# Optimization experiments

Hardware: AMD Instinct MI355X
Metric: run time of the kernel (lower is better)

Reference implementation:

```python
import jax, jax.numpy as jnp
import numpy as np

D_MODEL = 512
HIDDEN = 500
NEG_INF = -1e30


def setup_inputs() -> dict:
    key = jax.random.key(0)
    ks = jax.random.split(key, 12)
    N, K, d, L = 256, 1024, D_MODEL, 64
    s = 0.02
    return {
        "span_embs": jax.random.normal(ks[0], (N, d), jnp.float32),
        "knowledge_embs": jax.random.normal(ks[1], (K, d), jnp.float32),
        "span2concepts": jax.random.randint(ks[2], (N, L), 0, K, jnp.int32),
        "lengths": jax.random.randint(ks[3], (N,), 0, L, jnp.int32),
        "Ws": jax.random.normal(ks[4], (d, d), jnp.float32) * s,
        "bs": jnp.zeros((d,), jnp.float32),
        "W1": jax.random.normal(ks[5], (2 * d, HIDDEN), jnp.float32) * s,
        "b1": jnp.zeros((HIDDEN,), jnp.float32),
        "W2": jax.random.normal(ks[6], (HIDDEN, HIDDEN), jnp.float32) * s,
        "b2": jnp.zeros((HIDDEN,), jnp.float32),
        "W3": jax.random.normal(ks[7], (HIDDEN, 1), jnp.float32) * s,
        "b3": jnp.zeros((1,), jnp.float32),
    }


def reference(span_embs, knowledge_embs, span2concepts, lengths, Ws, bs, W1, b1, W2, b2, W3, b3):
    N, d = span_embs.shape
    K = knowledge_embs.shape[0]
    L = span2concepts.shape[1]

    # sentinel concept per candidate (row K of the per-candidate knowledge table)
    sentinel = jax.nn.relu(span_embs @ Ws + bs)  # [N, d]

    # FFNN scorer over concat([span, concept]) for all K+1 pairs.
    # Split W1 so the [N, K+1, 2d] concat is never materialized (same math).
    W1a, W1b = W1[:d], W1[d:]
    span_part = span_embs @ W1a                          # [N, HIDDEN]
    know_part = knowledge_embs @ W1b                     # [K, HIDDEN]
    sent_part = sentinel @ W1b                           # [N, HIDDEN]
    know_full_part = jnp.concatenate(
        [jnp.broadcast_to(know_part[None], (N, K, HIDDEN)), sent_part[:, None, :]], axis=1
    )                                                    # [N, K+1, HIDDEN]
    h = jax.nn.relu(span_part[:, None, :] + know_full_part + b1)
    h = jax.nn.relu(h @ W2 + b2)                         # [N, K+1, HIDDEN]
    scores = (h @ W3 + b3)[..., 0]                       # [N, K+1]

    # ragged gather: per-candidate concept list + sentinel index K, masked softmax
    valid = jnp.arange(L)[None, :] < jnp.maximum(lengths, 1)[:, None]          # [N, L]
    idx = jnp.concatenate([span2concepts, jnp.full((N, 1), K, jnp.int32)], axis=1)  # [N, L+1]
    mask = jnp.concatenate([valid, jnp.ones((N, 1), bool)], axis=1)            # [N, L+1]

    rel_scores = jnp.take_along_axis(scores, idx, axis=1)
    probs = jax.nn.softmax(jnp.where(mask, rel_scores, NEG_INF), axis=-1)      # [N, L+1]

    is_sent = (idx == K)[..., None]                                            # [N, L+1, 1]
    rel_embs = jnp.where(is_sent, sentinel[:, None, :],
                         knowledge_embs[jnp.minimum(idx, K - 1)])              # [N, L+1, d]
    features = jnp.einsum('nl,nld->nd', probs, rel_embs)                       # [N, d]
    return features, probs
```

## Files before the change

### kernel.cpp

```cpp
#include <hip/hip_runtime.h>
#include <math.h>
#include <stdint.h>

#define D 512
#define H 500
#define NSPAN 256
#define KCON 1024
#define L 64

typedef __attribute__((ext_vector_type(8))) short short8;
typedef __attribute__((ext_vector_type(4))) float floatx4;

__device__ __forceinline__ short f2bf(float f) {
    unsigned u = __builtin_bit_cast(unsigned, f);
    return (short)((u + 0x7fffu + ((u >> 16) & 1u)) >> 16);
}

__global__ __launch_bounds__(512) void k_prep(
    const float* __restrict__ W2, const float* __restrict__ Ws,
    const float* __restrict__ W1,
    short* __restrict__ W2bf, short* __restrict__ Wsbf,
    short* __restrict__ W1abf, short* __restrict__ W1bbf) {
    int b = blockIdx.x, tid = threadIdx.x;
    int mb = b >> 6;
    int s = (b & 63) * 512 + tid;
    int kq = s & 3, n = (s >> 2) & 511, kb = s >> 11;
    int k0 = kb * 32 + kq * 8;
    short8 v8;
    #pragma unroll
    for (int i = 0; i < 8; ++i) {
        int k = k0 + i;
        float v;
        if (mb == 0)      v = (k < H && n < H) ? W2[k * H + n] : 0.f;
        else if (mb == 1) v = Ws[k * D + n];
        else if (mb == 2) v = (n < H) ? W1[k * H + n] : 0.f;
        else              v = (n < H) ? W1[(D + k) * H + n] : 0.f;
        v8[i] = f2bf(v);
    }
    short* dst = (mb == 0) ? W2bf : (mb == 1) ? Wsbf : (mb == 2) ? W1abf : W1bbf;
    ((short8*)dst)[s] = v8;
}

__global__ __launch_bounds__(256) void k_mm1(
    const float* __restrict__ span, const float* __restrict__ know,
    const float* __restrict__ bs, const float* __restrict__ b1,
    const short* __restrict__ Wsbf, const short* __restrict__ W1abf,
    const short* __restrict__ W1bbf,
    float* __restrict__ spanb1, float* __restrict__ parts,
    float* __restrict__ sentinel) {
    __shared__ __align__(16) short Asw[16 * 512];
    int b = blockIdx.x, tid = threadIdx.x;
    int wv = tid >> 6, ln = tid & 63;
    int nl = ln & 15, kq = ln >> 4;
    int aoff = nl * 32 + kq * 8;

    if (b < 160) {
        int rg, nh;
        const float* src;
        const short8* B;
        bool is_span = (b < 32);
        if (is_span) { rg = b >> 1; nh = b & 1; src = span + rg * 16 * D;
                       B = (const short8*)W1abf; }
        else { int bb = b - 32; rg = bb >> 1; nh = bb & 1; src = know + rg * 16 * D;
               B = (const short8*)W1bbf; }
        {
            int r = tid >> 4, kb = tid & 15;
            const float* sp = src + r * D + kb * 32;
            short* dst = &Asw[kb * 512 + r * 32];
            #pragma unroll
            for (int i = 0; i < 32; ++i) dst[i] = f2bf(sp[i]);
        }
        __syncthreads();
        floatx4 acc[4];
        #pragma unroll
        for (int t = 0; t < 4; ++t) acc[t] = (floatx4){0.f, 0.f, 0.f, 0.f};
        int tb = nh * 16 + wv * 4;
        int boff = tb * 64 + nl * 4 + kq;
        #pragma unroll 1
        for (int kb = 0; kb < 16; ++kb) {
            short8 a = *(const short8*)&Asw[kb * 512 + aoff];
            short8 bf[4];
            #pragma unroll
            for (int t = 0; t < 4; ++t) bf[t] = B[kb * 2048 + boff + t * 64];
            #pragma unroll
            for (int t = 0; t < 4; ++t)
                acc[t] = __builtin_amdgcn_mfma_f32_16x16x32_bf16(a, bf[t], acc[t], 0, 0, 0);
        }
        #pragma unroll
        for (int t = 0; t < 4; ++t) {
            int col = (tb + t) * 16 + nl;
            if (col < H) {
                if (is_span) {
                    float bc = b1[col];
                    #pragma unroll
                    for (int r = 0; r < 4; ++r)
                        spanb1[(size_t)(rg * 16 + kq * 4 + r) * H + col] = acc[t][r] + bc;
                } else {
                    #pragma unroll
                    for (int r = 0; r < 4; ++r)
                        parts[(size_t)(rg * 16 + kq * 4 + r) * H + col] = acc[t][r];
                }
            }
        }
        return;
    }

    int rg = b - 160;
    const float* src = span + rg * 16 * D;
    {
        int r = tid >> 4, kb = tid & 15;
        const float* sp = src + r * D + kb * 32;
        short* dst = &Asw[kb * 512 + r * 32];
        #pragma unroll
        for (int i = 0; i < 32; ++i) dst[i] = f2bf(sp[i]);
    }
    __syncthreads();
    floatx4 acc[8];
    #pragma unroll
    for (int t = 0; t < 8; ++t) acc[t] = (floatx4){0.f, 0.f, 0.f, 0.f};
    int boff = wv * 8 * 64 + nl * 4 + kq;
    const short8* B1 = (const short8*)Wsbf;
    #pragma unroll 1
    for (int kb = 0; kb < 16; ++kb) {
        short8 a = *(const short8*)&Asw[kb * 512 + aoff];
        short8 bf[8];
        #pragma unroll
        for (int t = 0; t < 8; ++t) bf[t] = B1[kb * 2048 + boff + t * 64];
        #pragma unroll
        for (int t = 0; t < 8; ++t)
            acc[t] = __builtin_amdgcn_mfma_f32_16x16x32_bf16(a, bf[t], acc[t], 0, 0, 0);
    }
    float vbuf[8][4];
    #pragma unroll
    for (int t = 0; t < 8; ++t) {
        int col = (wv * 8 + t) * 16 + nl;
        float bc = bs[col];
        #pragma unroll
        for (int r = 0; r < 4; ++r) {
            float v = fmaxf(acc[t][r] + bc, 0.f);
            vbuf[t][r] = v;
            sentinel[(size_t)(rg * 16 + kq * 4 + r) * D + col] = v;
        }
    }
    __syncthreads();
    #pragma unroll
    for (int t = 0; t < 8; ++t) {
        int col = (wv * 8 + t) * 16 + nl;
        short* d = &Asw[(col >> 5) * 512 + (col & 31)];
        #pragma unroll
        for (int r = 0; r < 4; ++r) d[(kq * 4 + r) * 32] = f2bf(vbuf[t][r]);
    }
    __syncthreads();
    const short8* B2 = (const short8*)W1bbf;
    #pragma unroll
    for (int t = 0; t < 8; ++t) acc[t] = (floatx4){0.f, 0.f, 0.f, 0.f};
    #pragma unroll 1
    for (int kb = 0; kb < 16; ++kb) {
        short8 a = *(const short8*)&Asw[kb * 512 + aoff];
        short8 bf[8];
        #pragma unroll
        for (int t = 0; t < 8; ++t) bf[t] = B2[kb * 2048 + boff + t * 64];
        #pragma unroll
        for (int t = 0; t < 8; ++t)
            acc[t] = __builtin_amdgcn_mfma_f32_16x16x32_bf16(a, bf[t], acc[t], 0, 0, 0);
    }
    #pragma unroll
    for (int t = 0; t < 8; ++t) {
        int col = (wv * 8 + t) * 16 + nl;
        if (col < H) {
            #pragma unroll
            for (int r = 0; r < 4; ++r)
                parts[(size_t)(KCON + rg * 16 + kq * 4 + r) * H + col] = acc[t][r];
        }
    }
}

__global__ __launch_bounds__(512) void k_fused(
    const int* __restrict__ s2c, const int* __restrict__ lengths,
    const float* __restrict__ spanb1, const float* __restrict__ parts,
    const float* __restrict__ sentinel, const short* __restrict__ W2bf,
    const float* __restrict__ b2, const float* __restrict__ W3,
    const float* __restrict__ b3, const float* __restrict__ know,
    float* __restrict__ out_features, float* __restrict__ out_probs) {
    int n = blockIdx.x, tid = threadIdx.x;
    int V = lengths[n];
    V = (V < 1) ? 1 : ((V > 63) ? 63 : V);
    int R = V + 1;
    int nmt = (R + 15) >> 4;

    __shared__ __align__(16) short Asw[16 * 2048];
    __shared__ float red[8][64];
    __shared__ float sscore[64];
    __shared__ float p[L + 1];
    __shared__ int idx[L];
    __shared__ __align__(16) float4 partb[4][128];

    if (tid < L) idx[tid] = s2c[n * L + tid];

    {
        int r = tid >> 4, kb = tid & 15, k0 = kb * 32;
        const float* spn = spanb1 + (size_t)n * H;
        #pragma unroll
        for (int half = 0; half < 2; ++half) {
            int rr = r + half * 32;
            if (rr < nmt * 16) {
                int mt = rr >> 4, m = rr & 15;
                short* dst = &Asw[kb * 2048 + mt * 512 + m * 32];
                if (rr < R) {
                    const float* src = (rr < V)
                        ? parts + (size_t)s2c[n * L + rr] * H
                        : parts + (size_t)(KCON + n) * H;
                    const float4* s4 = (const float4*)(spn + k0);
                    const float4* r4 = (const float4*)(src + k0);
                    #pragma unroll
                    for (int g = 0; g < 8; ++g) {
                        if (k0 + g * 4 < H) {
                            float4 a = s4[g], c = r4[g];
                            dst[g * 4 + 0] = f2bf(fmaxf(a.x + c.x, 0.f));
                            dst[g * 4 + 1] = f2bf(fmaxf(a.y + c.y, 0.f));
                            dst[g * 4 + 2] = f2bf(fmaxf(a.z + c.z, 0.f));
                            dst[g * 4 + 3] = f2bf(fmaxf(a.w + c.w, 0.f));
                        } else {
                            dst[g * 4 + 0] = 0; dst[g * 4 + 1] = 0;
                            dst[g * 4 + 2] = 0; dst[g * 4 + 3] = 0;
                        }
                    }
                } else {
                    #pragma unroll
                    for (int g = 0; g < 8; ++g)
                        *(short4*)&dst[g * 4] = (short4){0, 0, 0, 0};
                }
            }
        }
    }
    __syncthreads();

    int wv = tid >> 6, ln = tid & 63;
    int nl = ln & 15, kq = ln >> 4;
    int aoffb = nl * 32 + kq * 8;
    int boffb = wv * 4 * 64 + nl * 4 + kq;
    floatx4 acc[4][4];
    #pragma unroll
    for (int mt = 0; mt < 4; ++mt)
        #pragma unroll
        for (int t = 0; t < 4; ++t) acc[mt][t] = (floatx4){0.f, 0.f, 0.f, 0.f};

    const short8* B = (const short8*)W2bf;
    #pragma unroll 1
    for (int kb = 0; kb < 16; ++kb) {
        short8 bfr[4];
        #pragma unroll
        for (int t = 0; t < 4; ++t) bfr[t] = B[kb * 2048 + boffb + t * 64];
        #pragma unroll
        for (int mt = 0; mt < 4; ++mt) {
            if (mt < nmt) {
                short8 a = *(const short8*)&Asw[kb * 2048 + mt * 512 + aoffb];
                #pragma unroll
                for (int t = 0; t < 4; ++t)
                    acc[mt][t] = __builtin_amdgcn_mfma_f32_16x16x32_bf16(a, bfr[t], acc[mt][t], 0, 0, 0);
            }
        }
    }

    float b2c[4], w3c[4];
    #pragma unroll
    for (int t = 0; t < 4; ++t) {
        int col = wv * 64 + t * 16 + nl;
        b2c[t] = (col < H) ? b2[col] : 0.f;
        w3c[t] = (col < H) ? W3[col] : 0.f;
    }
    #pragma unroll
    for (int mt = 0; mt < 4; ++mt) {
        if (mt < nmt) {
            #pragma unroll
            for (int r = 0; r < 4; ++r) {
                float v = fmaxf(acc[mt][0][r] + b2c[0], 0.f) * w3c[0]
                        + fmaxf(acc[mt][1][r] + b2c[1], 0.f) * w3c[1]
                        + fmaxf(acc[mt][2][r] + b2c[2], 0.f) * w3c[2]
                        + fmaxf(acc[mt][3][r] + b2c[3], 0.f) * w3c[3];
                v += __shfl_xor(v, 1, 64);
                v += __shfl_xor(v, 2, 64);
                v += __shfl_xor(v, 4, 64);
                v += __shfl_xor(v, 8, 64);
                if (nl == 0) red[wv][mt * 16 + kq * 4 + r] = v;
            }
        }
    }
    __syncthreads();
    if (tid < R) {
        float s = b3[0];
        #pragma unroll
        for (int w = 0; w < 8; ++w) s += red[w][tid];
        sscore[tid] = s;
    }
    __syncthreads();

    if (tid < 64) {
        float sV = sscore[V];
        float val = (tid < V) ? sscore[tid] : -1e30f;
        float m = val;
        #pragma unroll
        for (int off = 32; off > 0; off >>= 1) m = fmaxf(m, __shfl_xor(m, off, 64));
        m = fmaxf(m, sV);
        float e = (tid < V) ? expf(val - m) : 0.f;
        float s = e;
        #pragma unroll
        for (int off = 32; off > 0; off >>= 1) s += __shfl_xor(s, off, 64);
        float eL = expf(sV - m);
        float inv = 1.f / (s + eL);
        p[tid] = e * inv;
        if (tid == 0) p[L] = eL * inv;
    }
    __syncthreads();
    if (tid <= L) out_probs[n * (L + 1) + tid] = p[tid];

    int sub = tid >> 7, c = tid & 127;
    float4 acc4 = {0.f, 0.f, 0.f, 0.f};
    if (sub == 0) {
        float ps = p[L];
        float4 sv = ((const float4*)sentinel)[n * 128 + c];
        acc4.x = ps * sv.x; acc4.y = ps * sv.y; acc4.z = ps * sv.z; acc4.w = ps * sv.w;
    }
    const float4* kn = (const float4*)know;
    for (int l = sub; l < V; l += 4) {
        float pl = p[l];
        float4 v = kn[idx[l] * 128 + c];
        acc4.x = fmaf(pl, v.x, acc4.x); acc4.y = fmaf(pl, v.y, acc4.y);
        acc4.z = fmaf(pl, v.z, acc4.z); acc4.w = fmaf(pl, v.w, acc4.w);
    }
    partb[sub][c] = acc4;
    __syncthreads();
    if (tid < 128) {
        float4 a0 = partb[0][tid], a1 = partb[1][tid];
        float4 a2 = partb[2][tid], a3 = partb[3][tid];
        float4 o;
        o.x = a0.x + a1.x + a2.x + a3.x;
        o.y = a0.y + a1.y + a2.y + a3.y;
        o.z = a0.z + a1.z + a2.z + a3.z;
        o.w = a0.w + a1.w + a2.w + a3.w;
        ((float4*)out_features)[n * 128 + tid] = o;
    }
}

extern "C" void kernel_launch(void* const* d_in, const int* in_sizes, int n_in,
                              void* d_out, int out_size, void* d_ws, size_t ws_size,
                              hipStream_t stream) {
    const float* span = (const float*)d_in[0];
    const float* know = (const float*)d_in[1];
    const int* s2c = (const int*)d_in[2];
    const int* lengths = (const int*)d_in[3];
    const float* Ws = (const float*)d_in[4];
    const float* bs = (const float*)d_in[5];
    const float* W1 = (const float*)d_in[6];
    const float* b1 = (const float*)d_in[7];
    const float* W2 = (const float*)d_in[8];
    const float* b2 = (const float*)d_in[9];
    const float* W3 = (const float*)d_in[10];
    const float* b3 = (const float*)d_in[11];

    float* ws = (float*)d_ws;
    float* spanb1 = ws;
    float* parts = spanb1 + NSPAN * H;
    float* sentinel = parts + (KCON + NSPAN) * H;
    short* W2bf = (short*)(((uintptr_t)(sentinel + NSPAN * D) + 63) & ~(uintptr_t)63);
    short* Wsbf = W2bf + 512 * 512;
    short* W1abf = Wsbf + 512 * 512;
    short* W1bbf = W1abf + 512 * 512;

    float* out_features = (float*)d_out;
    float* out_probs = out_features + NSPAN * D;

    k_prep<<<256, 512, 0, stream>>>(W2, Ws, W1, W2bf, Wsbf, W1abf, W1bbf);
    k_mm1<<<176, 256, 0, stream>>>(span, know, bs, b1, Wsbf, W1abf, W1bbf,
                                   spanb1, parts, sentinel);
    k_fused<<<NSPAN, 512, 0, stream>>>(s2c, lengths, spanb1, parts, sentinel,
                                       W2bf, b2, W3, b3, know,
                                       out_features, out_probs);
}
```

Before: 126.7 us.

## Fuse three kernels into one cooperative kernel with grid-wide syncs

Replaces the prep, first-matmul and fused scoring kernels with a single cooperative kernel of 256 blocks that uses grid.sync between phases. This removes two kernel launch gaps. The mm1 phase is re-tiled to use 512 threads, so each wave now handles fewer column tiles, and the fp32 loads are vectorized as float4. The trade-off is the cost of grid-wide barriers, plus a shared-memory union sized for the largest phase, which may limit occupancy.

After: 299.0 us. 136% more time.

```diff
diff --git a/kernel.cpp b/kernel.cpp
--- a/kernel.cpp
+++ b/kernel.cpp
@@ -1,6 +1,9 @@
 #include <hip/hip_runtime.h>
+#include <hip/hip_cooperative_groups.h>
 #include <math.h>
 #include <stdint.h>
+
+namespace cg = cooperative_groups;
 
 #define D 512
 #define H 500
@@ -16,329 +19,331 @@
     return (short)((u + 0x7fffu + ((u >> 16) & 1u)) >> 16);
 }
 
-__global__ __launch_bounds__(512) void k_prep(
-    const float* __restrict__ W2, const float* __restrict__ Ws,
-    const float* __restrict__ W1,
+struct SharedMem {
+    union {
+        struct {
+            short Asw[16 * 2048];
+            float red[8][64];
+            float sscore[64];
+            float p[L + 1];
+            int idx[L];
+            float4 partb[4][128];
+        } f;
+        struct {
+            short Asw[16 * 512];
+        } m;
+    } u;
+};
+
+__global__ void __launch_bounds__(512) k_all(
+    const float* __restrict__ span, const float* __restrict__ know,
+    const int* __restrict__ s2c, const int* __restrict__ lengths,
+    const float* __restrict__ Ws, const float* __restrict__ bs,
+    const float* __restrict__ W1, const float* __restrict__ b1,
+    const float* __restrict__ W2, const float* __restrict__ b2,
+    const float* __restrict__ W3, const float* __restrict__ b3,
+    float* __restrict__ spanb1, float* __restrict__ parts,
+    float* __restrict__ sentinel,
     short* __restrict__ W2bf, short* __restrict__ Wsbf,
-    short* __restrict__ W1abf, short* __restrict__ W1bbf) {
-    int b = blockIdx.x, tid = threadIdx.x;
-    int mb = b >> 6;
-    int s = (b & 63) * 512 + tid;
-    int kq = s & 3, n = (s >> 2) & 511, kb = s >> 11;
-    int k0 = kb * 32 + kq * 8;
-    short8 v8;
-    #pragma unroll
-    for (int i = 0; i < 8; ++i) {
-        int k = k0 + i;
-        float v;
-        if (mb == 0)      v = (k < H && n < H) ? W2[k * H + n] : 0.f;
-        else if (mb == 1) v = Ws[k * D + n];
-        else if (mb == 2) v = (n < H) ? W1[k * H + n] : 0.f;
-        else              v = (n < H) ? W1[(D + k) * H + n] : 0.f;
-        v8[i] = f2bf(v);
-    }
-    short* dst = (mb == 0) ? W2bf : (mb == 1) ? Wsbf : (mb == 2) ? W1abf : W1bbf;
-    ((short8*)dst)[s] = v8;
-}
-
-__global__ __launch_bounds__(256) void k_mm1(
-    const float* __restrict__ span, const float* __restrict__ know,
-    const float* __restrict__ bs, const float* __restrict__ b1,
-    const short* __restrict__ Wsbf, const short* __restrict__ W1abf,
-    const short* __restrict__ W1bbf,
-    float* __restrict__ spanb1, float* __restrict__ parts,
-    float* __restrict__ sentinel) {
-    __shared__ __align__(16) short Asw[16 * 512];
+    short* __restrict__ W1abf, short* __restrict__ W1bbf,
+    float* __restrict__ out_features, float* __restrict__ out_probs) {
+    cg::grid_group grid = cg::this_grid();
+    __shared__ SharedMem sh;
     int b = blockIdx.x, tid = threadIdx.x;
     int wv = tid >> 6, ln = tid & 63;
     int nl = ln & 15, kq = ln >> 4;
-    int aoff = nl * 32 + kq * 8;
-
-    if (b < 160) {
-        int rg, nh;
+
+    {
+        int mb = b >> 6;
+        int s = (b & 63) * 512 + tid;
+        int skq = s & 3, n = (s >> 2) & 511, kb = s >> 11;
+        int k0 = kb * 32 + skq * 8;
+        short8 v8;
+        #pragma unroll
+        for (int i = 0; i < 8; ++i) {
+            int k = k0 + i;
+            float v;
+            if (mb == 0)      v = (k < H && n < H) ? W2[k * H + n] : 0.f;
+            else if (mb == 1) v = Ws[k * D + n];
+            else if (mb == 2) v = (n < H) ? W1[k * H + n] : 0.f;
+            else              v = (n < H) ? W1[(D + k) * H + n] : 0.f;
+            v8[i] = f2bf(v);
+        }
+        short* dst = (mb == 0) ? W2bf : (mb == 1) ? Wsbf : (mb == 2) ? W1abf : W1bbf;
+        ((short8*)dst)[s] = v8;
+    }
+    __threadfence();
+    grid.sync();
+
+    if (b < 176) {
+        short* Asw = sh.u.m.Asw;
         const float* src;
-        const short8* B;
-        bool is_span = (b < 32);
-        if (is_span) { rg = b >> 1; nh = b & 1; src = span + rg * 16 * D;
-                       B = (const short8*)W1abf; }
-        else { int bb = b - 32; rg = bb >> 1; nh = bb & 1; src = know + rg * 16 * D;
-               B = (const short8*)W1bbf; }
+        int rg, nh = 0, mode;
+        if (b < 32) { mode = 0; rg = b >> 1; nh = b & 1; src = span + rg * 16 * D; }
+        else if (b < 160) { mode = 1; int bb = b - 32; rg = bb >> 1; nh = bb & 1;
+                            src = know + rg * 16 * D; }
+        else { mode = 2; rg = b - 160; src = span + rg * 16 * D; }
+
         {
-            int r = tid >> 4, kb = tid & 15;
-            const float* sp = src + r * D + kb * 32;
-            short* dst = &Asw[kb * 512 + r * 32];
-            #pragma unroll
-            for (int i = 0; i < 32; ++i) dst[i] = f2bf(sp[i]);
-        }
-        __syncthreads();
-        floatx4 acc[4];
+            int r = tid >> 5, kh = tid & 31;
+            const float4* sp = (const float4*)(src + r * D + kh * 16);
+            short* dst = &Asw[(kh >> 1) * 512 + r * 32 + (kh & 1) * 16];
+            #pragma unroll
+            for (int g = 0; g < 4; ++g) {
+                float4 a = sp[g];
+                short4 o = {f2bf(a.x), f2bf(a.y), f2bf(a.z), f2bf(a.w)};
+                ((short4*)dst)[g] = o;
+            }
+        }
+        __syncthreads();
+        int aoff = nl * 32 + kq * 8;
+
+        if (mode < 2) {
+            const short8* B = (const short8*)((mode == 0) ? W1abf : W1bbf);
+            int tb = nh * 16 + wv * 2;
+            int boff = tb * 64 + nl * 4 + kq;
+            floatx4 acc[2];
+            acc[0] = (floatx4){0.f, 0.f, 0.f, 0.f};
+            acc[1] = acc[0];
+            #pragma unroll 1
+            for (int kb = 0; kb < 16; ++kb) {
+                short8 a = *(const short8*)&Asw[kb * 512 + aoff];
+                short8 bf0 = B[kb * 2048 + boff];
+                short8 bf1 = B[kb * 2048 + boff + 64];
+                acc[0] = __builtin_amdgcn_mfma_f32_16x16x32_bf16(a, bf0, acc[0], 0, 0, 0);
+                acc[1] = __builtin_amdgcn_mfma_f32_16x16x32_bf16(a, bf1, acc[1], 0, 0, 0);
+            }
+            #pragma unroll
+            for (int t = 0; t < 2; ++t) {
+                int col = (tb + t) * 16 + nl;
+                if (col < H) {
+                    if (mode == 0) {
+                        float bc = b1[col];
+                        #pragma unroll
+                        for (int r = 0; r < 4; ++r)
+                            spanb1[(size_t)(rg * 16 + kq * 4 + r) * H + col] = acc[t][r] + bc;
+                    } else {
+                        #pragma unroll
+                        for (int r = 0; r < 4; ++r)
+                            parts[(size_t)(rg * 16 + kq * 4 + r) * H + col] = acc[t][r];
+                    }
+                }
+            }
+        } else {
+            int boff = (wv * 4) * 64 + nl * 4 + kq;
+            floatx4 acc[4];
+            #pragma unroll
+            for (int t = 0; t < 4; ++t) acc[t] = (floatx4){0.f, 0.f, 0.f, 0.f};
+            const short8* B1 = (const short8*)Wsbf;
+            #pragma unroll 1
+            for (int kb = 0; kb < 16; ++kb) {
+                short8 a = *(const short8*)&Asw[kb * 512 + aoff];
+                short8 bf[4];
+                #pragma unroll
+                for (int t = 0; t < 4; ++t) bf[t] = B1[kb * 2048 + boff + t * 64];
+                #pragma unroll
+                for (int t = 0; t < 4; ++t)
+                    acc[t] = __builtin_amdgcn_mfma_f32_16x16x32_bf16(a, bf[t], acc[t], 0, 0, 0);
+            }
+            float vbuf[4][4];
+            #pragma unroll
+            for (int t = 0; t < 4; ++t) {
+                int col = (wv * 4 + t) * 16 + nl;
+                float bc = bs[col];
+                #pragma unroll
+                for (int r = 0; r < 4; ++r) {
+                    float v = fmaxf(acc[t][r] + bc, 0.f);
+                    vbuf[t][r] = v;
+                    sentinel[(size_t)(rg * 16 + kq * 4 + r) * D + col] = v;
+                }
+            }
+            __syncthreads();
+            #pragma unroll
+            for (int t = 0; t < 4; ++t) {
+                int col = (wv * 4 + t) * 16 + nl;
+                short* d = &Asw[(col >> 5) * 512 + (col & 31)];
+                #pragma unroll
+                for (int r = 0; r < 4; ++r) d[(kq * 4 + r) * 32] = f2bf(vbuf[t][r]);
+            }
+            __syncthreads();
+            const short8* B2 = (const short8*)W1bbf;
+            #pragma unroll
+            for (int t = 0; t < 4; ++t) acc[t] = (floatx4){0.f, 0.f, 0.f, 0.f};
+            #pragma unroll 1
+            for (int kb = 0; kb < 16; ++kb) {
+                short8 a = *(const short8*)&Asw[kb * 512 + aoff];
+                short8 bf[4];
+                #pragma unroll
+                for (int t = 0; t < 4; ++t) bf[t] = B2[kb * 2048 + boff + t * 64];
+                #pragma unroll
+                for (int t = 0; t < 4; ++t)
+                    acc[t] = __builtin_amdgcn_mfma_f32_16x16x32_bf16(a, bf[t], acc[t], 0, 0, 0);
+            }
+            #pragma unroll
+            for (int t = 0; t < 4; ++t) {
+                int col = (wv * 4 + t) * 16 + nl;
+                if (col < H) {
+                    #pragma unroll
+                    for (int r = 0; r < 4; ++r)
+                        parts[(size_t)(KCON + rg * 16 + kq * 4 + r) * H + col] = acc[t][r];
+                }
+            }
+        }
+    }
+    __threadfence();
+    grid.sync();
+
+    {
+        int n = b;
+        int V = lengths[n];
+        V = (V < 1) ? 1 : ((V > 63) ? 63 : V);
+        int R = V + 1;
+        int nmt = (R + 15) >> 4;
+
+        short* Asw = sh.u.f.Asw;
+        if (tid < L) sh.u.f.idx[tid] = s2c[n * L + tid];
+
+        {
+            int r = tid >> 4, kb = tid & 15, k0 = kb * 32;
+            const float* spn = spanb1 + (size_t)n * H;
+            #pragma unroll
+            for (int half = 0; half < 2; ++half) {
+                int rr = r + half * 32;
+                if (rr < nmt * 16) {
+                    int mt = rr >> 4, m = rr & 15;
+                    short* dst = &Asw[kb * 2048 + mt * 512 + m * 32];
+                    if (rr < R) {
+                        const float* src = (rr < V)
+                            ? parts + (size_t)s2c[n * L + rr] * H
+                            : parts + (size_t)(KCON + n) * H;
+                        const float4* s4 = (const float4*)(spn + k0);
+                        const float4* r4 = (const float4*)(src + k0);
+                        #pragma unroll
+                        for (int g = 0; g < 8; ++g) {
+                            if (k0 + g * 4 < H) {
+                                float4 a = s4[g], c = r4[g];
+                                dst[g * 4 + 0] = f2bf(fmaxf(a.x + c.x, 0.f));
+                                dst[g * 4 + 1] = f2bf(fmaxf(a.y + c.y, 0.f));
+                                dst[g * 4 + 2] = f2bf(fmaxf(a.z + c.z, 0.f));
+                                dst[g * 4 + 3] = f2bf(fmaxf(a.w + c.w, 0.f));
+                            } else {
+                                *(short4*)&dst[g * 4] = (short4){0, 0, 0, 0};
+                            }
+                        }
+                    } else {
+                        #pragma unroll
+                        for (int g = 0; g < 8; ++g)
+                            *(short4*)&dst[g * 4] = (short4){0, 0, 0, 0};
+                    }
+                }
+            }
+        }
+        __syncthreads();
+
+        int aoffb = nl * 32 + kq * 8;
+        int boffb = wv * 4 * 64 + nl * 4 + kq;
+        floatx4 acc[4][4];
         #pragma unroll
-        for (int t = 0; t < 4; ++t) acc[t] = (floatx4){0.f, 0.f, 0.f, 0.f};
-        int tb = nh * 16 + wv * 4;
-        int boff = tb * 64 + nl * 4 + kq;
+        for (int mt = 0; mt < 4; ++mt)
+            #pragma unroll
+            for (int t = 0; t < 4; ++t) acc[mt][t] = (floatx4){0.f, 0.f, 0.f, 0.f};
+
+        const short8* B = (const short8*)W2bf;
         #pragma unroll 1
         for (int kb = 0; kb < 16; ++kb) {
-            short8 a = *(const short8*)&Asw[kb * 512 + aoff];
-            short8 bf[4];
-            #pragma unroll
-            for (int t = 0; t < 4; ++t) bf[t] = B[kb * 2048 + boff + t * 64];
-            #pragma unroll
-            for (int t = 0; t < 4; ++t)
-                acc[t] = __builtin_amdgcn_mfma_f32_16x16x32_bf16(a, bf[t], acc[t], 0, 0, 0);
-        }
+            short8 bfr[4];
+            #pragma unroll
+            for (int t = 0; t < 4; ++t) bfr[t] = B[kb * 2048 + boffb + t * 64];
+            #pragma unroll
+            for (int mt = 0; mt < 4; ++mt) {
+                if (mt < nmt) {
+                    short8 a = *(const short8*)&Asw[kb * 2048 + mt * 512 + aoffb];
+                    #pragma unroll
+                    for (int t = 0; t < 4; ++t)
+                        acc[mt][t] = __builtin_amdgcn_mfma_f32_16x16x32_bf16(a, bfr[t], acc[mt][t], 0, 0, 0);
+                }
+            }
+        }
+
+        float b2c[4], w3c[4];
         #pragma unroll
         for (int t = 0; t < 4; ++t) {
-            int col = (tb + t) * 16 + nl;
-            if (col < H) {
-                if (is_span) {
-                    float bc = b1[col];
-                    #pragma unroll
-                    for (int r = 0; r < 4; ++r)
-                        spanb1[(size_t)(rg * 16 + kq * 4 + r) * H + col] = acc[t][r] + bc;
-                } else {
-                    #pragma unroll
-                    for (int r = 0; r < 4; ++r)
-                        parts[(size_t)(rg * 16 + kq * 4 + r) * H + col] = acc[t][r];
-                }
-            }
-        }
-        return;
-    }
-
-    int rg = b - 160;
-    const float* src = span + rg * 16 * D;
-    {
-        int r = tid >> 4, kb = tid & 15;
-        const float* sp = src + r * D + kb * 32;
-        short* dst = &Asw[kb * 512 + r * 32];
-        #pragma unroll
-        for (int i = 0; i < 32; ++i) dst[i] = f2bf(sp[i]);
-    }
-    __syncthreads();
-    floatx4 acc[8];
-    #pragma unroll
-    for (int t = 0; t < 8; ++t) acc[t] = (floatx4){0.f, 0.f, 0.f, 0.f};
-    int boff = wv * 8 * 64 + nl * 4 + kq;
-    const short8* B1 = (const short8*)Wsbf;
-    #pragma unroll 1
-    for (int kb = 0; kb < 16; ++kb) {
-        short8 a = *(const short8*)&Asw[kb * 512 + aoff];
-        short8 bf[8];
-        #pragma unroll
-        for (int t = 0; t < 8; ++t) bf[t] = B1[kb * 2048 + boff + t * 64];
-        #pragma unroll
-        for (int t = 0; t < 8; ++t)
-            acc[t] = __builtin_amdgcn_mfma_f32_16x16x32_bf16(a, bf[t], acc[t], 0, 0, 0);
-    }
-    float vbuf[8][4];
-    #pragma unroll
-    for (int t = 0; t < 8; ++t) {
-        int col = (wv * 8 + t) * 16 + nl;
-        float bc = bs[col];
-        #pragma unroll
-        for (int r = 0; r < 4; ++r) {
-            float v = fmaxf(acc[t][r] + bc, 0.f);
-            vbuf[t][r] = v;
-            sentinel[(size_t)(rg * 16 + kq * 4 + r) * D + col] = v;
-        }
-    }
-    __syncthreads();
-    #pragma unroll
-    for (int t = 0; t < 8; ++t) {
-        int col = (wv * 8 + t) * 16 + nl;
-        short* d = &Asw[(col >> 5) * 512 + (col & 31)];
-        #pragma unroll
-        for (int r = 0; r < 4; ++r) d[(kq * 4 + r) * 32] = f2bf(vbuf[t][r]);
-    }
-    __syncthreads();
-    const short8* B2 = (const short8*)W1bbf;
-    #pragma unroll
-    for (int t = 0; t < 8; ++t) acc[t] = (floatx4){0.f, 0.f, 0.f, 0.f};
-    #pragma unroll 1
-    for (int kb = 0; kb < 16; ++kb) {
-        short8 a = *(const short8*)&Asw[kb * 512 + aoff];
-        short8 bf[8];
-        #pragma unroll
-        for (int t = 0; t < 8; ++t) bf[t] = B2[kb * 2048 + boff + t * 64];
-        #pragma unroll
-        for (int t = 0; t < 8; ++t)
-            acc[t] = __builtin_amdgcn_mfma_f32_16x16x32_bf16(a, bf[t], acc[t], 0, 0, 0);
-    }
-    #pragma unroll
-    for (int t = 0; t < 8; ++t) {
-        int col = (wv * 8 + t) * 16 + nl;
-        if (col < H) {
-            #pragma unroll
-            for (int r = 0; r < 4; ++r)
-                parts[(size_t)(KCON + rg * 16 + kq * 4 + r) * H + col] = acc[t][r];
-        }
-    }
-}
-
-__global__ __launch_bounds__(512) void k_fused(
-    const int* __restrict__ s2c, const int* __restrict__ lengths,
-    const float* __restrict__ spanb1, const float* __restrict__ parts,
-    const float* __restrict__ sentinel, const short* __restrict__ W2bf,
-    const float* __restrict__ b2, const float* __restrict__ W3,
-    const float* __restrict__ b3, const float* __restrict__ know,
-    float* __restrict__ out_features, float* __restrict__ out_probs) {
-    int n = blockIdx.x, tid = threadIdx.x;
-    int V = lengths[n];
-    V = (V < 1) ? 1 : ((V > 63) ? 63 : V);
-    int R = V + 1;
-    int nmt = (R + 15) >> 4;
-
-    __shared__ __align__(16) short Asw[16 * 2048];
-    __shared__ float red[8][64];
-    __shared__ float sscore[64];
-    __shared__ float p[L + 1];
-    __shared__ int idx[L];
-    __shared__ __align__(16) float4 partb[4][128];
-
-    if (tid < L) idx[tid] = s2c[n * L + tid];
-
-    {
-        int r = tid >> 4, kb = tid & 15, k0 = kb * 32;
-        const float* spn = spanb1 + (size_t)n * H;
-        #pragma unroll
-        for (int half = 0; half < 2; ++half) {
-            int rr = r + half * 32;
-            if (rr < nmt * 16) {
-                int mt = rr >> 4, m = rr & 15;
-                short* dst = &Asw[kb * 2048 + mt * 512 + m * 32];
-                if (rr < R) {
-                    const float* src = (rr < V)
-                        ? parts + (size_t)s2c[n * L + rr] * H
-                        : parts + (size_t)(KCON + n) * H;
-                    const float4* s4 = (const float4*)(spn + k0);
-                    const float4* r4 = (const float4*)(src + k0);
-                    #pragma unroll
-                    for (int g = 0; g < 8; ++g) {
-                        if (k0 + g * 4 < H) {
-                            float4 a = s4[g], c = r4[g];
-                            dst[g * 4 + 0] = f2bf(fmaxf(a.x + c.x, 0.f));
-                            dst[g * 4 + 1] = f2bf(fmaxf(a.y + c.y, 0.f));
-                            dst[g * 4 + 2] = f2bf(fmaxf(a.z + c.z, 0.f));
-                            dst[g * 4 + 3] = f2bf(fmaxf(a.w + c.w, 0.f));
-                        } else {
-                            dst[g * 4 + 0] = 0; dst[g * 4 + 1] = 0;
-                            dst[g * 4 + 2] = 0; dst[g * 4 + 3] = 0;
-                        }
-                    }
-                } else {
-                    #pragma unroll
-                    for (int g = 0; g < 8; ++g)
-                        *(short4*)&dst[g * 4] = (short4){0, 0, 0, 0};
-                }
-            }
-        }
-    }
-    __syncthreads();
-
-    int wv = tid >> 6, ln = tid & 63;
-    int nl = ln & 15, kq = ln >> 4;
-    int aoffb = nl * 32 + kq * 8;
-    int boffb = wv * 4 * 64 + nl * 4 + kq;
-    floatx4 acc[4][4];
-    #pragma unroll
-    for (int mt = 0; mt < 4; ++mt)
-        #pragma unroll
-        for (int t = 0; t < 4; ++t) acc[mt][t] = (floatx4){0.f, 0.f, 0.f, 0.f};
-
-    const short8* B = (const short8*)W2bf;
-    #pragma unroll 1
-    for (int kb = 0; kb < 16; ++kb) {
-        short8 bfr[4];
-        #pragma unroll
-        for (int t = 0; t < 4; ++t) bfr[t] = B[kb * 2048 + boffb + t * 64];
+            int col = wv * 64 + t * 16 + nl;
+            b2c[t] = (col < H) ? b2[col] : 0.f;
+            w3c[t] = (col < H) ? W3[col] : 0.f;
+        }
         #pragma unroll
         for (int mt = 0; mt < 4; ++mt) {
             if (mt < nmt) {
-                short8 a = *(const short8*)&Asw[kb * 2048 + mt * 512 + aoffb];
-                #pragma unroll
-                for (int t = 0; t < 4; ++t)
-                    acc[mt][t] = __builtin_amdgcn_mfma_f32_16x16x32_bf16(a, bfr[t], acc[mt][t], 0, 0, 0);
-            }
-        }
-    }
-
-    float b2c[4], w3c[4];
-    #pragma unroll
-    for (int t = 0; t < 4; ++t) {
-        int col = wv * 64 + t * 16 + nl;
-        b2c[t] = (col < H) ? b2[col] : 0.f;
-        w3c[t] = (col < H) ? W3[col] : 0.f;
-    }
-    #pragma unroll
-    for (int mt = 0; mt < 4; ++mt) {
-        if (mt < nmt) {
-            #pragma unroll
-            for (int r = 0; r < 4; ++r) {
-                float v = fmaxf(acc[mt][0][r] + b2c[0], 0.f) * w3c[0]
-                        + fmaxf(acc[mt][1][r] + b2c[1], 0.f) * w3c[1]
-                        + fmaxf(acc[mt][2][r] + b2c[2], 0.f) * w3c[2]
-                        + fmaxf(acc[mt][3][r] + b2c[3], 0.f) * w3c[3];
-                v += __shfl_xor(v, 1, 64);
-                v += __shfl_xor(v, 2, 64);
-                v += __shfl_xor(v, 4, 64);
-                v += __shfl_xor(v, 8, 64);
-                if (nl == 0) red[wv][mt * 16 + kq * 4 + r] = v;
-            }
-        }
-    }
-    __syncthreads();
-    if (tid < R) {
-        float s = b3[0];
-        #pragma unroll
-        for (int w = 0; w < 8; ++w) s += red[w][tid];
-        sscore[tid] = s;
-    }
-    __syncthreads();
-
-    if (tid < 64) {
-        float sV = sscore[V];
-        float val = (tid < V) ? sscore[tid] : -1e30f;
-        float m = val;
-        #pragma unroll
-        for (int off = 32; off > 0; off >>= 1) m = fmaxf(m, __shfl_xor(m, off, 64));
-        m = fmaxf(m, sV);
-        float e = (tid < V) ? expf(val - m) : 0.f;
-        float s = e;
-        #pragma unroll
-        for (int off = 32; off > 0; off >>= 1) s += __shfl_xor(s, off, 64);
-        float eL = expf(sV - m);
-        float inv = 1.f / (s + eL);
-        p[tid] = e * inv;
-        if (tid == 0) p[L] = eL * inv;
-    }
-    __syncthreads();
-    if (tid <= L) out_probs[n * (L + 1) + tid] = p[tid];
-
-    int sub = tid >> 7, c = tid & 127;
-    float4 acc4 = {0.f, 0.f, 0.f, 0.f};
-    if (sub == 0) {
-        float ps = p[L];
-        float4 sv = ((const float4*)sentinel)[n * 128 + c];
-        acc4.x = ps * sv.x; acc4.y = ps * sv.y; acc4.z = ps * sv.z; acc4.w = ps * sv.w;
-    }
-    const float4* kn = (const float4*)know;
-    for (int l = sub; l < V; l += 4) {
-        float pl = p[l];
-        float4 v = kn[idx[l] * 128 + c];
-        acc4.x = fmaf(pl, v.x, acc4.x); acc4.y = fmaf(pl, v.y, acc4.y);
-        acc4.z = fmaf(pl, v.z, acc4.z); acc4.w = fmaf(pl, v.w, acc4.w);
-    }
-    partb[sub][c] = acc4;
-    __syncthreads();
-    if (tid < 128) {
-        float4 a0 = partb[0][tid], a1 = partb[1][tid];
-        float4 a2 = partb[2][tid], a3 = partb[3][tid];
-        float4 o;
-        o.x = a0.x + a1.x + a2.x + a3.x;
-        o.y = a0.y + a1.y + a2.y + a3.y;
-        o.z = a0.z + a1.z + a2.z + a3.z;
-        o.w = a0.w + a1.w + a2.w + a3.w;
-        ((float4*)out_features)[n * 128 + tid] = o;
+                #pragma unroll
+                for (int r = 0; r < 4; ++r) {
+                    float v = fmaxf(acc[mt][0][r] + b2c[0], 0.f) * w3c[0]
+                            + fmaxf(acc[mt][1][r] + b2c[1], 0.f) * w3c[1]
+                            + fmaxf(acc[mt][2][r] + b2c[2], 0.f) * w3c[2]
+                            + fmaxf(acc[mt][3][r] + b2c[3], 0.f) * w3c[3];
+                    v += __shfl_xor(v, 1, 64);
+                    v += __shfl_xor(v, 2, 64);
+                    v += __shfl_xor(v, 4, 64);
+                    v += __shfl_xor(v, 8, 64);
+                    if (nl == 0) sh.u.f.red[wv][mt * 16 + kq * 4 + r] = v;
+                }
+            }
+        }
+        __syncthreads();
+        if (tid < R) {
+            float s = b3[0];
+            #pragma unroll
+            for (int w = 0; w < 8; ++w) s += sh.u.f.red[w][tid];
+            sh.u.f.sscore[tid] = s;
+        }
+        __syncthreads();
+
+        if (tid < 64) {
+            float sV = sh.u.f.sscore[V];
+            float val = (tid < V) ? sh.u.f.sscore[tid] : -1e30f;
+            float m = val;
+            #pragma unroll
+            for (int off = 32; off > 0; off >>= 1) m = fmaxf(m, __shfl_xor(m, off, 64));
+            m = fmaxf(m, sV);
+            float e = (tid < V) ? expf(val - m) : 0.f;
+            float s = e;
+            #pragma unroll
+            for (int off = 32; off > 0; off >>= 1) s += __shfl_xor(s, off, 64);
+            float eL = expf(sV - m);
+            float inv = 1.f / (s + eL);
+            sh.u.f.p[tid] = e * inv;
+            if (tid == 0) sh.u.f.p[L] = eL * inv;
+        }
+        __syncthreads();
+        if (tid <= L) out_probs[n * (L + 1) + tid] = sh.u.f.p[tid];
+
+        int sub = tid >> 7, c = tid & 127;
+        float4 acc4 = {0.f, 0.f, 0.f, 0.f};
+        if (sub == 0) {
+            float ps = sh.u.f.p[L];
+            float4 sv = ((const float4*)sentinel)[n * 128 + c];
+            acc4.x = ps * sv.x; acc4.y = ps * sv.y;
+            acc4.z = ps * sv.z; acc4.w = ps * sv.w;
+        }
+        const float4* kn = (const float4*)know;
+        for (int l = sub; l < V; l += 4) {
+            float pl = sh.u.f.p[l];
+            float4 v = kn[sh.u.f.idx[l] * 128 + c];
+            acc4.x = fmaf(pl, v.x, acc4.x); acc4.y = fmaf(pl, v.y, acc4.y);
+            acc4.z = fmaf(pl, v.z, acc4.z); acc4.w = fmaf(pl, v.w, acc4.w);
+        }
+        sh.u.f.partb[sub][c] = acc4;
+        __syncthreads();
+        if (tid < 128) {
+            float4 a0 = sh.u.f.partb[0][tid], a1 = sh.u.f.partb[1][tid];
+            float4 a2 = sh.u.f.partb[2][tid], a3 = sh.u.f.partb[3][tid];
+            float4 o;
+            o.x = a0.x + a1.x + a2.x + a3.x;
+            o.y = a0.y + a1.y + a2.y + a3.y;
+            o.z = a0.z + a1.z + a2.z + a3.z;
+            o.w = a0.w + a1.w + a2.w + a3.w;
+            ((float4*)out_features)[n * 128 + tid] = o;
+        }
     }
 }
 
@@ -358,8 +363,8 @@
     const float* W3 = (const float*)d_in[10];
     const float* b3 = (const float*)d_in[11];
 
-    float* ws = (float*)d_ws;
-    float* spanb1 = ws;
+    float* wsp = (float*)d_ws;
+    float* spanb1 = wsp;
     float* parts = spanb1 + NSPAN * H;
     float* sentinel = parts + (KCON + NSPAN) * H;
     short* W2bf = (short*)(((uintptr_t)(sentinel + NSPAN * D) + 63) & ~(uintptr_t)63);
@@ -370,10 +375,14 @@
     float* out_features = (float*)d_out;
     float* out_probs = out_features + NSPAN * D;
 
-    k_prep<<<256, 512, 0, stream>>>(W2, Ws, W1, W2bf, Wsbf, W1abf, W1bbf);
-    k_mm1<<<176, 256, 0, stream>>>(span, know, bs, b1, Wsbf, W1abf, W1bbf,
-                                   spanb1, parts, sentinel);
-    k_fused<<<NSPAN, 512, 0, stream>>>(s2c, lengths, spanb1, parts, sentinel,
-                                       W2bf, b2, W3, b3, know,
-                                       out_features, out_probs);
+    void* args[] = {
+        (void*)&span, (void*)&know, (void*)&s2c, (void*)&lengths,
+        (void*)&Ws, (void*)&bs, (void*)&W1, (void*)&b1,
+        (void*)&W2, (void*)&b2, (void*)&W3, (void*)&b3,
+        (void*)&spanb1, (void*)&parts, (void*)&sentinel,
+        (void*)&W2bf, (void*)&Wsbf, (void*)&W1abf, (void*)&W1bbf,
+        (void*)&out_features, (void*)&out_probs,
+    };
+    hipLaunchCooperativeKernel((void*)k_all, dim3(NSPAN), dim3(512), args, 0,
+                               stream);
 }
```

## Move W2 bf16 conversion into mm1 kernel and prefetch B fragments in MFMA loops

Applied to the files above, without the earlier changes.

Takes the W2-to-bf16 conversion out of the prep kernel and runs it in 128 extra blocks of the mm1 launch, so it overlaps with the first-layer GEMM instead of sitting on the critical path. Both the mm1 and fused W2 MFMA loops now double-buffer the B-fragment global loads, issuing the next k-block's loads before the current MFMAs. The tail zero-fill is also vectorised to a single short4 store. The prefetch adds register pressure, and it wraps around to issue one redundant load on the last iteration.

Result: no change. 125.2 us (-1.1%).

```diff
diff --git a/kernel.cpp b/kernel.cpp
--- a/kernel.cpp
+++ b/kernel.cpp
@@ -17,10 +17,9 @@
 }
 
 __global__ __launch_bounds__(512) void k_prep(
-    const float* __restrict__ W2, const float* __restrict__ Ws,
-    const float* __restrict__ W1,
-    short* __restrict__ W2bf, short* __restrict__ Wsbf,
-    short* __restrict__ W1abf, short* __restrict__ W1bbf) {
+    const float* __restrict__ Ws, const float* __restrict__ W1,
+    short* __restrict__ Wsbf, short* __restrict__ W1abf,
+    short* __restrict__ W1bbf) {
     int b = blockIdx.x, tid = threadIdx.x;
     int mb = b >> 6;
     int s = (b & 63) * 512 + tid;
@@ -31,25 +30,41 @@
     for (int i = 0; i < 8; ++i) {
         int k = k0 + i;
         float v;
-        if (mb == 0)      v = (k < H && n < H) ? W2[k * H + n] : 0.f;
-        else if (mb == 1) v = Ws[k * D + n];
-        else if (mb == 2) v = (n < H) ? W1[k * H + n] : 0.f;
+        if (mb == 0)      v = Ws[k * D + n];
+        else if (mb == 1) v = (n < H) ? W1[k * H + n] : 0.f;
         else              v = (n < H) ? W1[(D + k) * H + n] : 0.f;
         v8[i] = f2bf(v);
     }
-    short* dst = (mb == 0) ? W2bf : (mb == 1) ? Wsbf : (mb == 2) ? W1abf : W1bbf;
+    short* dst = (mb == 0) ? Wsbf : (mb == 1) ? W1abf : W1bbf;
     ((short8*)dst)[s] = v8;
 }
 
 __global__ __launch_bounds__(256) void k_mm1(
     const float* __restrict__ span, const float* __restrict__ know,
     const float* __restrict__ bs, const float* __restrict__ b1,
+    const float* __restrict__ W2,
     const short* __restrict__ Wsbf, const short* __restrict__ W1abf,
     const short* __restrict__ W1bbf,
     float* __restrict__ spanb1, float* __restrict__ parts,
-    float* __restrict__ sentinel) {
+    float* __restrict__ sentinel, short* __restrict__ W2bf) {
     __shared__ __align__(16) short Asw[16 * 512];
     int b = blockIdx.x, tid = threadIdx.x;
+
+    if (b >= 176) {
+        int s = (b - 176) * 256 + tid;
+        int kq = s & 3, n = (s >> 2) & 511, kb = s >> 11;
+        int k0 = kb * 32 + kq * 8;
+        short8 v8;
+        #pragma unroll
+        for (int i = 0; i < 8; ++i) {
+            int k = k0 + i;
+            float v = (k < H && n < H) ? W2[k * H + n] : 0.f;
+            v8[i] = f2bf(v);
+        }
+        ((short8*)W2bf)[s] = v8;
+        return;
+    }
+
     int wv = tid >> 6, ln = tid & 63;
     int nl = ln & 15, kq = ln >> 4;
     int aoff = nl * 32 + kq * 8;
@@ -76,15 +91,20 @@
         for (int t = 0; t < 4; ++t) acc[t] = (floatx4){0.f, 0.f, 0.f, 0.f};
         int tb = nh * 16 + wv * 4;
         int boff = tb * 64 + nl * 4 + kq;
+        short8 bcur[4], bnxt[4];
+        #pragma unroll
+        for (int t = 0; t < 4; ++t) bcur[t] = B[boff + t * 64];
         #pragma unroll 1
         for (int kb = 0; kb < 16; ++kb) {
+            int kn = (kb + 1) & 15;
+            #pragma unroll
+            for (int t = 0; t < 4; ++t) bnxt[t] = B[kn * 2048 + boff + t * 64];
             short8 a = *(const short8*)&Asw[kb * 512 + aoff];
-            short8 bf[4];
-            #pragma unroll
-            for (int t = 0; t < 4; ++t) bf[t] = B[kb * 2048 + boff + t * 64];
             #pragma unroll
             for (int t = 0; t < 4; ++t)
-                acc[t] = __builtin_amdgcn_mfma_f32_16x16x32_bf16(a, bf[t], acc[t], 0, 0, 0);
+                acc[t] = __builtin_amdgcn_mfma_f32_16x16x32_bf16(a, bcur[t], acc[t], 0, 0, 0);
+            #pragma unroll
+            for (int t = 0; t < 4; ++t) bcur[t] = bnxt[t];
         }
         #pragma unroll
         for (int t = 0; t < 4; ++t) {
@@ -221,8 +241,7 @@
                             dst[g * 4 + 2] = f2bf(fmaxf(a.z + c.z, 0.f));
                             dst[g * 4 + 3] = f2bf(fmaxf(a.w + c.w, 0.f));
                         } else {
-                            dst[g * 4 + 0] = 0; dst[g * 4 + 1] = 0;
-                            dst[g * 4 + 2] = 0; dst[g * 4 + 3] = 0;
+                            *(short4*)&dst[g * 4] = (short4){0, 0, 0, 0};
                         }
                     }
                 } else {
@@ -246,20 +265,25 @@
         for (int t = 0; t < 4; ++t) acc[mt][t] = (floatx4){0.f, 0.f, 0.f, 0.f};
 
     const short8* B = (const short8*)W2bf;
+    short8 bcur[4], bnxt[4];
+    #pragma unroll
+    for (int t = 0; t < 4; ++t) bcur[t] = B[boffb + t * 64];
     #pragma unroll 1
     for (int kb = 0; kb < 16; ++kb) {
-        short8 bfr[4];
-        #pragma unroll
-        for (int t = 0; t < 4; ++t) bfr[t] = B[kb * 2048 + boffb + t * 64];
+        int kn = (kb + 1) & 15;
+        #pragma unroll
+        for (int t = 0; t < 4; ++t) bnxt[t] = B[kn * 2048 + boffb + t * 64];
         #pragma unroll
         for (int mt = 0; mt < 4; ++mt) {
             if (mt < nmt) {
                 short8 a = *(const short8*)&Asw[kb * 2048 + mt * 512 + aoffb];
                 #pragma unroll
                 for (int t = 0; t < 4; ++t)
-                    acc[mt][t] = __builtin_amdgcn_mfma_f32_16x16x32_bf16(a, bfr[t], acc[mt][t], 0, 0, 0);
+                    acc[mt][t] = __builtin_amdgcn_mfma_f32_16x16x32_bf16(a, bcur[t], acc[mt][t], 0, 0, 0);
             }
         }
+        #pragma unroll
+        for (int t = 0; t < 4; ++t) bcur[t] = bnxt[t];
     }
 
     float b2c[4], w3c[4];
@@ -358,8 +382,8 @@
     const float* W3 = (const float*)d_in[10];
     const float* b3 = (const float*)d_in[11];
 
-    float* ws = (float*)d_ws;
-    float* spanb1 = ws;
+    float* wsp = (float*)d_ws;
+    float* spanb1 = wsp;
     float* parts = spanb1 + NSPAN * H;
     float* sentinel = parts + (KCON + NSPAN) * H;
     short* W2bf = (short*)(((uintptr_t)(sentinel + NSPAN * D) + 63) & ~(uintptr_t)63);
@@ -370,9 +394,9 @@
     float* out_features = (float*)d_out;
     float* out_probs = out_features + NSPAN * D;
 
-    k_prep<<<256, 512, 0, stream>>>(W2, Ws, W1, W2bf, Wsbf, W1abf, W1bbf);
-    k_mm1<<<176, 256, 0, stream>>>(span, know, bs, b1, Wsbf, W1abf, W1bbf,
-                                   spanb1, parts, sentinel);
+    k_prep<<<192, 512, 0, stream>>>(Ws, W1, Wsbf, W1abf, W1bbf);
+    k_mm1<<<304, 256, 0, stream>>>(span, know, bs, b1, W2, Wsbf, W1abf, W1bbf,
+                                   spanb1, parts, sentinel, W2bf);
     k_fused<<<NSPAN, 512, 0, stream>>>(s2c, lengths, spanb1, parts, sentinel,
                                        W2bf, b2, W3, b3, know,
                                        out_features, out_probs);
```
